# Optimization experiments

Measured on AMD Instinct MI355X. Metric: run time of the kernel, lower is better.

## Reference

```python
import jax, jax.numpy as jnp
import numpy as np

H = 768    # bert hidden size
P = 64     # num dialogue pairs
L = 2 * P  # interleaved (user,system) sequence length
C = 2      # num_classes (CRF tags)
LAM = 0.1  # lambda_mle


def setup_inputs():
    key = jax.random.key(0)
    ks = jax.random.split(key, 21)
    def rn(k, shape, s=0.05):
        return jax.random.normal(k, shape, dtype=jnp.float32) * s
    G = 4 * H
    return {
        "user_repr": rn(ks[0], (P, H), 1.0),
        "system_repr": rn(ks[1], (P, H), 1.0),
        "post_Wih0": rn(ks[2], (2, G, H)), "post_Whh0": rn(ks[3], (2, G, H)), "post_b0": rn(ks[4], (2, G)),
        "post_Wih1": rn(ks[5], (2, G, 2 * H)), "post_Whh1": rn(ks[6], (2, G, H)), "post_b1": rn(ks[7], (2, G)),
        "prior_Wih0": rn(ks[8], (2, G, H)), "prior_Whh0": rn(ks[9], (2, G, H)), "prior_b0": rn(ks[10], (2, G)),
        "prior_Wih1": rn(ks[11], (2, G, 2 * H)), "prior_Whh1": rn(ks[12], (2, G, H)), "prior_b1": rn(ks[13], (2, G)),
        "post_proj_W": rn(ks[14], (C, 2 * H)), "post_proj_b": rn(ks[15], (C,)),
        "prior_proj_W": rn(ks[16], (C, 2 * H)), "prior_proj_b": rn(ks[17], (C,)),
        "transitions": rn(ks[18], (C, C), 0.1),
        "user_I_label": jax.random.randint(ks[19], (1, P), 0, C),
        "system_I_label": jax.random.randint(ks[20], (1, P), 0, C),
    }


def _lstm_dir(x, mask, Wih, Whh, b, reverse):
    # x: [P, L, Din]; mask: [P, L] bool (True = valid step). Masked steps freeze state,
    # so each row computes the LSTM over its own prefix exactly as the per-pair loop does.
    Pn, Ln, _ = x.shape
    Hn = Whh.shape[1]
    xw = jnp.einsum('pld,gd->plg', x, Wih) + b  # [P, L, 4H] input projections (torch gate order i,f,g,o)
    def step(carry, inp):
        h, c = carry
        xw_t, m_t = inp
        gates = xw_t + h @ Whh.T
        i, f, g, o = jnp.split(gates, 4, axis=-1)
        c2 = jax.nn.sigmoid(f) * c + jax.nn.sigmoid(i) * jnp.tanh(g)
        h2 = jax.nn.sigmoid(o) * jnp.tanh(c2)
        m = m_t[:, None]
        h = jnp.where(m, h2, h)
        c = jnp.where(m, c2, c)
        return (h, c), h
    init = (jnp.zeros((Pn, Hn), x.dtype), jnp.zeros((Pn, Hn), x.dtype))
    _, hs = jax.lax.scan(step, init, (jnp.swapaxes(xw, 0, 1), mask.T), reverse=reverse)
    return jnp.swapaxes(hs, 0, 1)  # [P, L, H]


def _bilstm(x, mask, layers):
    for Wih, Whh, b in layers:
        fwd = _lstm_dir(x, mask, Wih[0], Whh[0], b[0], False)
        bwd = _lstm_dir(x, mask, Wih[1], Whh[1], b[1], True)
        x = jnp.concatenate([fwd, bwd], axis=-1)
    return x


def _forward(user_repr, system_repr,
             post_Wih0, post_Whh0, post_b0, post_Wih1, post_Whh1, post_b1,
             prior_Wih0, prior_Whh0, prior_b0, prior_Wih1, prior_Whh1, prior_b1,
             post_proj_W, post_proj_b, prior_proj_W, prior_proj_b, transitions, labs):
    seq = jnp.stack([user_repr, system_repr], axis=1).reshape(L, H)  # interleaved u0,s0,u1,s1,...
    l = 2 * (jnp.arange(P) + 1)                 # prefix length per pair
    t = jnp.arange(L)
    mask = t[None, :] < l[:, None]              # [P, L]
    xb = jnp.broadcast_to(seq[None], (P, L, H))
    # posterior branch: biLSTM over each prefix, then emissions
    post_out = _bilstm(xb, mask, [(post_Wih0, post_Whh0, post_b0), (post_Wih1, post_Whh1, post_b1)])
    em = post_out @ post_proj_W.T + post_proj_b  # [P, L, C]
    mf = mask.astype(em.dtype)
    # CRF gold score per pair
    e_lab = jnp.take_along_axis(em, jnp.broadcast_to(labs[None, :, None], (P, L, 1)), axis=2)[..., 0]
    trans_step = transitions[labs[:-1], labs[1:]]  # [L-1]
    gold = (e_lab * mf).sum(1) + (trans_step[None, :] * mf[:, 1:]).sum(1)
    # CRF forward algorithm (log partition), masked scan over time
    def fstep(alpha, inp):
        em_t, m_t = inp  # [P, C], [P]
        new = jax.nn.logsumexp(alpha[:, :, None] + transitions[None, :, :] + em_t[:, None, :], axis=1)
        return jnp.where(m_t[:, None], new, alpha), None
    alpha, _ = jax.lax.scan(fstep, em[:, 0, :], (jnp.swapaxes(em[:, 1:, :], 0, 1), mask[:, 1:].T))
    total = jax.nn.logsumexp(alpha, axis=1)
    loss_crf = jnp.mean(total - gold)
    # prior branch: prefix minus last token, take last valid hidden
    mask_p = t[None, :] < (l - 1)[:, None]
    prior_out = _bilstm(xb, mask_p, [(prior_Wih0, prior_Whh0, prior_b0), (prior_Wih1, prior_Whh1, prior_b1)])
    prior_last = jnp.take_along_axis(prior_out, jnp.broadcast_to((l - 2)[:, None, None], (P, 1, 2 * H)), axis=1)[:, 0, :]
    prior_emis = prior_last @ prior_proj_W.T + prior_proj_b  # [P, C]
    post_last = jnp.take_along_axis(em, jnp.broadcast_to((l - 1)[:, None, None], (P, 1, C)), axis=1)[:, 0, :]
    loss_mle = jnp.mean((prior_emis - jax.lax.stop_gradient(post_last)) ** 2)
    return loss_crf, loss_mle, loss_crf + LAM * loss_mle


def reference(user_repr, system_repr,
              post_Wih0, post_Whh0, post_b0, post_Wih1, post_Whh1, post_b1,
              prior_Wih0, prior_Whh0, prior_b0, prior_Wih1, prior_Whh1, prior_b1,
              post_proj_W, post_proj_b, prior_proj_W, prior_proj_b, transitions,
              user_I_label, system_I_label):
    labs = jnp.stack([user_I_label[0], system_I_label[0]], axis=1).reshape(L)
    return _forward(user_repr, system_repr,
                    post_Wih0, post_Whh0, post_b0, post_Wih1, post_Whh1, post_b1,
                    prior_Wih0, prior_Whh0, prior_b0, prior_Wih1, prior_Whh1, prior_b1,
                    post_proj_W, post_proj_b, prior_proj_W, prior_proj_b, transitions, labs)
```

## Files before the change

kernel.cpp:

```cpp
#include <hip/hip_runtime.h>


typedef short v8s __attribute__((ext_vector_type(8)));
typedef float v4f __attribute__((ext_vector_type(4)));
typedef unsigned short u16;

#define MFMA(a, b, c) __builtin_amdgcn_mfma_f32_16x16x32_bf16((a), (b), (c), 0, 0, 0)

static constexpr size_t WMAT    = (size_t)96 * 3072 * 8;
static constexpr size_t SLOT64  = (size_t)96 * 64 * 8;
static constexpr size_t SLOT16  = (size_t)96 * 16 * 8;
static constexpr size_t SLOT128 = (size_t)96 * 128 * 8;

static constexpr size_t OFF_CALL = 0;
static constexpr size_t SZ_CALL  = (size_t)8 * 64 * 768 * 4;
static constexpr size_t OFF_EM   = OFF_CALL + SZ_CALL;
static constexpr size_t SZ_EM    = (size_t)2 * 64 * 128 * 2 * 4;
static constexpr size_t OFF_XW0  = OFF_EM + SZ_EM;
static constexpr size_t SZ_XW    = (size_t)4 * 128 * 3072 * 4;
static constexpr size_t OFF_XW1  = OFF_XW0 + SZ_XW;
static constexpr size_t OFF_SEQ  = OFF_XW1 + SZ_XW;
static constexpr size_t SZ_SEQ   = (size_t)96 * 128 * 8 * 2;
static constexpr size_t OFF_LABS = OFF_SEQ + SZ_SEQ;
static constexpr size_t SZ_LABS  = 512;
static constexpr size_t OFF_W0   = OFF_LABS + SZ_LABS;
static constexpr size_t SZ_W4    = (size_t)4 * WMAT * 2;
static constexpr size_t OFF_W1X  = OFF_W0 + SZ_W4;
static constexpr size_t OFF_W1R  = OFF_W1X + SZ_W4;
static constexpr size_t OFF_F0   = OFF_W1R + SZ_W4;
static constexpr size_t SZ_F0    = (size_t)2 * 129 * SLOT16 * 2;
static constexpr size_t OFF_H0F  = OFF_F0 + SZ_F0;
static constexpr size_t SZ_H0F   = (size_t)2 * SLOT128 * 2;
static constexpr size_t OFF_B0   = OFF_H0F + SZ_H0F;
static constexpr size_t SZ_S64   = (size_t)2 * 129 * SLOT64 * 2;
static constexpr size_t OFF_F1   = OFF_B0 + SZ_S64;
static constexpr size_t OFF_B1   = OFF_F1 + SZ_S64;
static constexpr size_t WS_NEED  = OFF_B1 + SZ_S64;

static __device__ __forceinline__ u16 f2b(float f) {
  unsigned int u = __float_as_uint(f);
  unsigned int r = (u + 0x7FFFu + ((u >> 16) & 1u)) >> 16;
  return (u16)r;
}
static __device__ __forceinline__ float b2f(u16 u) {
  return __uint_as_float(((unsigned int)u) << 16);
}
static __device__ __forceinline__ float sigf(float x) {
  return 1.0f / (1.0f + __expf(-x));
}
static __device__ __forceinline__ float tanhfast(float x) {
  return 1.0f - 2.0f / (__expf(2.0f * x) + 1.0f);
}
static __device__ __forceinline__ float lse2(float a, float b) {
  float mx = fmaxf(a, b);
  return mx + __logf(__expf(a - mx) + __expf(b - mx));
}

static __device__ __forceinline__ void stage_w(const u16* mat, int kb0, int jb, u16* lds) {
  const int4* src = (const int4*)mat;
  int4* dst = (int4*)lds;
  int tid = threadIdx.x;
#pragma unroll
  for (int it = 0; it < 12; ++it) {
    int ck = it * 256 + tid;
    int kb = ck >> 6;
    int r = ck & 63;
    int g = (r >> 4) * 768 + jb + (r & 15);
    dst[ck] = src[(size_t)(kb0 + kb) * 3072 + g];
  }
}

__global__ void init_zero(float* c_all, u16* f0a, u16* f0b, u16* b0a, u16* b0b,
                          u16* f1a, u16* f1b, u16* b1a, u16* b1b) {
  int idx = blockIdx.x * 256 + threadIdx.x;
  c_all[idx] = 0.0f;
  if (idx < (int)SLOT16) { f0a[idx] = 0; f0b[idx] = 0; }
  if (idx < (int)SLOT64) {
    b0a[idx] = 0; b0b[idx] = 0;
    f1a[idx] = 0; f1b[idx] = 0;
    b1a[idx] = 0; b1b[idx] = 0;
  }
}

__global__ void build_seq(const float* user, const float* sysr, const int* ulab,
                          const int* slab, u16* seqkp, int* labs) {
  int idx = blockIdx.x * 256 + threadIdx.x;
  int t = idx / 768;
  int hh = idx - t * 768;
  float v = (t & 1) ? sysr[(t >> 1) * 768 + hh] : user[(t >> 1) * 768 + hh];
  seqkp[((size_t)(hh >> 3) * 128 + t) * 8 + (hh & 7)] = f2b(v);
  if (idx < 128) labs[idx] = (idx & 1) ? slab[idx >> 1] : ulab[idx >> 1];
}

__global__ void cvt_w(const float* postWhh0, const float* priWhh0,
                      const float* postWih1, const float* priWih1,
                      const float* postWhh1, const float* priWhh1,
                      u16* W0kp, u16* W1xkp, u16* W1rkp) {
  int mat = blockIdx.y;
  int grp = mat >> 2;
  int sub = mat & 3;
  int m = sub >> 1;
  int dirw = sub & 1;
  const float* src;
  int stride, coff;
  u16* dstb;
  if (grp == 0)      { src = m ? priWhh0 : postWhh0; stride = 768;  coff = 0;   dstb = W0kp; }
  else if (grp == 1) { src = m ? priWih1 : postWih1; stride = 1536; coff = 768; dstb = W1xkp; }
  else               { src = m ? priWhh1 : postWhh1; stride = 768;  coff = 0;   dstb = W1rkp; }
  src += (size_t)dirw * 3072 * stride;
  int cid = blockIdx.x * 256 + threadIdx.x;
  int g = cid / 96;
  int kb = cid - g * 96;
  const float* s = src + (size_t)g * stride + coff + (size_t)kb * 8;
  union { u16 h[8]; int4 v; } u;
#pragma unroll
  for (int j = 0; j < 8; ++j) u.h[j] = f2b(s[j]);
  ((int4*)(dstb + (size_t)sub * WMAT))[(size_t)kb * 3072 + g] = u.v;
}

__global__ void __launch_bounds__(256) xw_gemm(const u16* Akp, unsigned long long Astride,
                                               const float* Wm0, const float* Wm1, int wstride,
                                               const float* bm0, const float* bm1, float* out) {
  __shared__ u16 lds[48 * 64 * 8];
  int tid = threadIdx.x;
  int lane = tid & 63;
  int wave = tid >> 6;
  int md = blockIdx.y;
  int m = md >> 1;
  int dir = md & 1;
  const u16* A = Akp + (size_t)m * Astride;
  const float* W = (m ? Wm1 : Wm0) + (size_t)dir * 3072 * wstride;
  const float* b = (m ? bm1 : bm0) + dir * 3072;
  int g0 = blockIdx.x * 64;
  int quad = lane >> 4, l15 = lane & 15;
  v4f acc[2][4];
#pragma unroll
  for (int a = 0; a < 2; ++a)
#pragma unroll
    for (int nt = 0; nt < 4; ++nt) acc[a][nt] = (v4f){0.f, 0.f, 0.f, 0.f};

  for (int hfl = 0; hfl < 2; ++hfl) {
    if (hfl) __syncthreads();
    for (int it = 0; it < 12; ++it) {
      int ck = it * 256 + tid;
      int kb = ck >> 6;
      int r = ck & 63;
      int g = g0 + r;
      const float* s = W + (size_t)g * wstride + (size_t)(hfl * 48 + kb) * 8;
      union { u16 h[8]; int4 v; } u;
#pragma unroll
      for (int j = 0; j < 8; ++j) u.h[j] = f2b(s[j]);
      *(int4*)(lds + (size_t)ck * 8) = u.v;
    }
    __syncthreads();
    for (int lt = 0; lt < 12; ++lt) {
      int kblk = (hfl * 12 + lt) * 4 + quad;
      v8s a0 = ((const v8s*)A)[(size_t)kblk * 128 + (wave * 2 + 0) * 16 + l15];
      v8s a1 = ((const v8s*)A)[(size_t)kblk * 128 + (wave * 2 + 1) * 16 + l15];
#pragma unroll
      for (int nt = 0; nt < 4; ++nt) {
        v8s bb = *(const v8s*)(lds + ((size_t)((lt * 4 + quad) * 64) + nt * 16 + l15) * 8);
        acc[0][nt] = MFMA(a0, bb, acc[0][nt]);
        acc[1][nt] = MFMA(a1, bb, acc[1][nt]);
      }
    }
  }
#pragma unroll
  for (int a = 0; a < 2; ++a)
#pragma unroll
    for (int nt = 0; nt < 4; ++nt) {
      int g = g0 + nt * 16 + l15;
      float bv = b[g];
#pragma unroll
      for (int r = 0; r < 4; ++r) {
        int trow = (wave * 2 + a) * 16 + quad * 4 + r;
        out[(size_t)(md * 128 + trow) * 3072 + g] = acc[a][nt][r] + bv;
      }
    }
}

__global__ void __launch_bounds__(256) stepA_k(int t, const u16* W0kp, const float* xw0,
                                               u16* B0, u16* F0, u16* h0f, float* c_all) {
  __shared__ u16 lds[48 * 64 * 8];
  int tid = threadIdx.x;
  int lane = tid & 63;
  int wave = tid >> 6;
  int c = blockIdx.y;
  int isf = c >> 1;
  int m = c & 1;
  int dir = isf ? 0 : 1;
  int jb = blockIdx.x * 16;
  int quad = lane >> 4, l15 = lane & 15;
  const u16* mat = W0kp + (size_t)(m * 2 + dir) * WMAT;
  const u16* Asrc;
  int R, rowbase;
  if (isf) { Asrc = F0 + (size_t)(m * 129 + t) * SLOT16; R = 16; rowbase = 0; }
  else     { Asrc = B0 + (size_t)(m * 129 + t + 1) * SLOT64; R = 64; rowbase = wave * 16; }
  v4f acc[4];
#pragma unroll
  for (int gt = 0; gt < 4; ++gt) acc[gt] = (v4f){0.f, 0.f, 0.f, 0.f};
  bool docomp = (!isf) || (wave == 0);

  for (int hfl = 0; hfl < 2; ++hfl) {
    if (hfl) __syncthreads();
    stage_w(mat, hfl * 48, jb, lds);
    __syncthreads();
    if (docomp) {
      for (int lt = 0; lt < 12; ++lt) {
        int kblk = hfl * 48 + lt * 4 + quad;
        v8s a = ((const v8s*)Asrc)[(size_t)kblk * R + rowbase + l15];
#pragma unroll
        for (int gt = 0; gt < 4; ++gt) {
          v8s bb = *(const v8s*)(lds + ((size_t)((lt * 4 + quad) * 4 + gt) * 16 + l15) * 8);
          acc[gt] = MFMA(a, bb, acc[gt]);
        }
      }
    }
  }
  if (!docomp) return;

  int j = jb + l15;
  const float* xw = xw0 + (size_t)((m * 2 + dir) * 128 + t) * 3072;
  float xi = xw[j], xf = xw[768 + j], xg = xw[1536 + j], xo = xw[2304 + j];
  float* cs = c_all + (size_t)c * 64 * 768;
  if (!isf) {
    u16* dst = B0 + (size_t)(m * 129 + t) * SLOT64;
#pragma unroll
    for (int r = 0; r < 4; ++r) {
      int p = wave * 16 + quad * 4 + r;
      float gi = sigf(acc[0][r] + xi), gf = sigf(acc[1][r] + xf);
      float gg = tanhfast(acc[2][r] + xg), go = sigf(acc[3][r] + xo);
      float cold = cs[(size_t)p * 768 + j];
      float cn = gf * cold + gi * gg;
      float hn = go * tanhfast(cn);
      int lenp = 2 * p + 2 - m;
      bool act = t < lenp;
      float ce = act ? cn : 0.f;
      float he = act ? hn : 0.f;
      cs[(size_t)p * 768 + j] = ce;
      dst[((size_t)(j >> 3) * 64 + p) * 8 + (j & 7)] = f2b(he);
    }
  } else {
    if (quad == 0) {
      float gi = sigf(acc[0][0] + xi), gf = sigf(acc[1][0] + xf);
      float gg = tanhfast(acc[2][0] + xg), go = sigf(acc[3][0] + xo);
      float cold = cs[j];
      float cn = gf * cold + gi * gg;
      float hn = go * tanhfast(cn);
      cs[j] = cn;
      F0[(size_t)(m * 129 + t + 1) * SLOT16 + ((size_t)(j >> 3) * 16) * 8 + (j & 7)] = f2b(hn);
      h0f[(size_t)m * SLOT128 + ((size_t)(j >> 3) * 128 + t) * 8 + (j & 7)] = f2b(hn);
    }
  }
}

__global__ void __launch_bounds__(256) stepB_k(int t, const u16* W1x, const u16* W1r,
                                               const float* xw1s, const u16* B0, u16* F1,
                                               u16* B1, float* c_all) {
  __shared__ u16 lds[48 * 64 * 8];
  int tid = threadIdx.x;
  int lane = tid & 63;
  int wave = tid >> 6;
  int md = blockIdx.y;
  int m = md >> 1;
  int dir = md & 1;
  int jb = blockIdx.x * 16;
  int quad = lane >> 4, l15 = lane & 15;
  const u16* A1 = B0 + (size_t)(m * 129 + t) * SLOT64;
  const u16* A2 = dir ? (const u16*)(B1 + (size_t)(m * 129 + t + 1) * SLOT64)
                      : (const u16*)(F1 + (size_t)(m * 129 + t) * SLOT64);
  v4f acc[4];
#pragma unroll
  for (int gt = 0; gt < 4; ++gt) acc[gt] = (v4f){0.f, 0.f, 0.f, 0.f};

  for (int q = 0; q < 4; ++q) {
    if (q) __syncthreads();
    const u16* mat = (q < 2 ? W1x : W1r) + (size_t)md * WMAT;
    stage_w(mat, (q & 1) * 48, jb, lds);
    __syncthreads();
    const u16* As = (q < 2) ? A1 : A2;
    int akb0 = (q & 1) * 48;
    for (int lt = 0; lt < 12; ++lt) {
      v8s a = ((const v8s*)As)[(size_t)(akb0 + lt * 4 + quad) * 64 + wave * 16 + l15];
#pragma unroll
      for (int gt = 0; gt < 4; ++gt) {
        v8s bb = *(const v8s*)(lds + ((size_t)((lt * 4 + quad) * 4 + gt) * 16 + l15) * 8);
        acc[gt] = MFMA(a, bb, acc[gt]);
      }
    }
  }

  int j = jb + l15;
  const float* xw = xw1s + (size_t)(md * 128 + t) * 3072;
  float xi = xw[j], xf = xw[768 + j], xg = xw[1536 + j], xo = xw[2304 + j];
  float* cs = c_all + (size_t)(4 + md) * 64 * 768;
  u16* dst = dir ? (B1 + (size_t)(m * 129 + t) * SLOT64)
                 : (F1 + (size_t)(m * 129 + t + 1) * SLOT64);
  const u16* F1t = F1 + (size_t)(m * 129 + t) * SLOT64;
#pragma unroll
  for (int r = 0; r < 4; ++r) {
    int p = wave * 16 + quad * 4 + r;
    float gi = sigf(acc[0][r] + xi), gf = sigf(acc[1][r] + xf);
    float gg = tanhfast(acc[2][r] + xg), go = sigf(acc[3][r] + xo);
    float cold = cs[(size_t)p * 768 + j];
    float cn = gf * cold + gi * gg;
    float hn = go * tanhfast(cn);
    int lenp = 2 * p + 2 - m;
    bool act = t < lenp;
    float he, ce;
    if (!dir) {
      if (act) { he = hn; ce = cn; }
      else { he = b2f(F1t[((size_t)(j >> 3) * 64 + p) * 8 + (j & 7)]); ce = cold; }
    } else {
      he = act ? hn : 0.f;
      ce = act ? cn : 0.f;
    }
    cs[(size_t)p * 768 + j] = ce;
    dst[((size_t)(j >> 3) * 64 + p) * 8 + (j & 7)] = f2b(he);
  }
}

__global__ void __launch_bounds__(256) em_k(const u16* F1, const u16* B1,
                                            const float* pW0, const float* pb0,
                                            const float* pW1, const float* pb1, float* em) {
  int wid = blockIdx.x * 4 + (threadIdx.x >> 6);
  int lane = threadIdx.x & 63;
  int m = wid >> 13;
  int rem = wid & 8191;
  int p = rem >> 7;
  int t = rem & 127;
  const u16* hf = F1 + (size_t)(m * 129 + t + 1) * SLOT64;
  const u16* hb = B1 + (size_t)(m * 129 + t) * SLOT64;
  const float* Pw = m ? pW1 : pW0;
  const float* Pb = m ? pb1 : pb0;
  float s0 = 0.f, s1 = 0.f;
#pragma unroll
  for (int i = 0; i < 12; ++i) {
    int j = i * 64 + lane;
    size_t o = ((size_t)(j >> 3) * 64 + p) * 8 + (j & 7);
    float vf = b2f(hf[o]);
    float vb = b2f(hb[o]);
    s0 += Pw[j] * vf + Pw[768 + j] * vb;
    s1 += Pw[1536 + j] * vf + Pw[2304 + j] * vb;
  }
  for (int off = 32; off; off >>= 1) {
    s0 += __shfl_down(s0, off, 64);
    s1 += __shfl_down(s1, off, 64);
  }
  if (lane == 0) {
    em[((size_t)(m * 64 + p) * 128 + t) * 2 + 0] = s0 + Pb[0];
    em[((size_t)(m * 64 + p) * 128 + t) * 2 + 1] = s1 + Pb[1];
  }
}

__global__ void final_k(const float* em, const int* labs, const float* T, float* out) {
  int p = threadIdx.x;
  const float* emP = em + (size_t)p * 128 * 2;
  int lp = 2 * p + 2;
  float T00 = T[0], T01 = T[1], T10 = T[2], T11 = T[3];
  int prevlab = labs[0];
  float gold = emP[prevlab];
  for (int t = 1; t < lp; ++t) {
    int lb = labs[t];
    gold += emP[t * 2 + lb] + (prevlab ? (lb ? T11 : T10) : (lb ? T01 : T00));
    prevlab = lb;
  }
  float a0 = emP[0], a1 = emP[1];
  for (int t = 1; t < lp; ++t) {
    float n0 = lse2(a0 + T00, a1 + T10) + emP[t * 2];
    float n1 = lse2(a0 + T01, a1 + T11) + emP[t * 2 + 1];
    a0 = n0;
    a1 = n1;
  }
  float crf = lse2(a0, a1) - gold;
  const float* emR = em + (size_t)(64 + p) * 128 * 2;
  int lpr = 2 * p + 1;
  float d0 = emR[(lpr - 1) * 2 + 0] - emP[(lp - 1) * 2 + 0];
  float d1 = emR[(lpr - 1) * 2 + 1] - emP[(lp - 1) * 2 + 1];
  float mse = d0 * d0 + d1 * d1;
  for (int off = 32; off; off >>= 1) {
    crf += __shfl_down(crf, off, 64);
    mse += __shfl_down(mse, off, 64);
  }
  if (p == 0) {
    float lc = crf / 64.f;
    float lm = mse / 128.f;
    out[0] = lc;
    out[1] = lm;
    out[2] = lc + 0.1f * lm;
  }
}

extern "C" void kernel_launch(void* const* d_in, const int* in_sizes, int n_in,
                              void* d_out, int out_size, void* d_ws, size_t ws_size,
                              hipStream_t stream) {
  (void)in_sizes; (void)n_in; (void)out_size;
  if (ws_size < WS_NEED) return;

  const float* user     = (const float*)d_in[0];
  const float* sysr     = (const float*)d_in[1];
  const float* postWih0 = (const float*)d_in[2];
  const float* postWhh0 = (const float*)d_in[3];
  const float* postb0   = (const float*)d_in[4];
  const float* postWih1 = (const float*)d_in[5];
  const float* postWhh1 = (const float*)d_in[6];
  const float* postb1   = (const float*)d_in[7];
  const float* priWih0  = (const float*)d_in[8];
  const float* priWhh0  = (const float*)d_in[9];
  const float* prib0    = (const float*)d_in[10];
  const float* priWih1  = (const float*)d_in[11];
  const float* priWhh1  = (const float*)d_in[12];
  const float* prib1    = (const float*)d_in[13];
  const float* postPW   = (const float*)d_in[14];
  const float* postPb   = (const float*)d_in[15];
  const float* priPW    = (const float*)d_in[16];
  const float* priPb    = (const float*)d_in[17];
  const float* trans    = (const float*)d_in[18];
  const int*   ulab     = (const int*)d_in[19];
  const int*   slab     = (const int*)d_in[20];
  float* out = (float*)d_out;

  char* w = (char*)d_ws;
  float* c_all = (float*)(w + OFF_CALL);
  float* em    = (float*)(w + OFF_EM);
  float* xw0   = (float*)(w + OFF_XW0);
  float* xw1s  = (float*)(w + OFF_XW1);
  u16* seqkp   = (u16*)(w + OFF_SEQ);
  int* labs    = (int*)(w + OFF_LABS);
  u16* W0kp    = (u16*)(w + OFF_W0);
  u16* W1xkp   = (u16*)(w + OFF_W1X);
  u16* W1rkp   = (u16*)(w + OFF_W1R);
  u16* F0      = (u16*)(w + OFF_F0);
  u16* h0f     = (u16*)(w + OFF_H0F);
  u16* B0      = (u16*)(w + OFF_B0);
  u16* F1      = (u16*)(w + OFF_F1);
  u16* B1      = (u16*)(w + OFF_B1);

  init_zero<<<1536, 256, 0, stream>>>(
      c_all,
      F0, F0 + (size_t)129 * SLOT16,
      B0 + (size_t)128 * SLOT64, B0 + (size_t)(129 + 128) * SLOT64,
      F1, F1 + (size_t)129 * SLOT64,
      B1 + (size_t)128 * SLOT64, B1 + (size_t)(129 + 128) * SLOT64);

  build_seq<<<384, 256, 0, stream>>>(user, sysr, ulab, slab, seqkp, labs);

  cvt_w<<<dim3(1152, 12), 256, 0, stream>>>(postWhh0, priWhh0, postWih1, priWih1,
                                            postWhh1, priWhh1, W0kp, W1xkp, W1rkp);

  xw_gemm<<<dim3(48, 4), 256, 0, stream>>>(seqkp, 0ULL, postWih0, priWih0, 768,
                                           postb0, prib0, xw0);

  for (int t = 0; t < 128; ++t)
    stepA_k<<<dim3(48, 4), 256, 0, stream>>>(t, W0kp, xw0, B0, F0, h0f, c_all);

  xw_gemm<<<dim3(48, 4), 256, 0, stream>>>(h0f, (unsigned long long)SLOT128,
                                           postWih1, priWih1, 1536, postb1, prib1, xw1s);

  for (int t = 0; t < 128; ++t)
    stepB_k<<<dim3(48, 4), 256, 0, stream>>>(t, W1xkp, W1rkp, xw1s, B0, F1, B1, c_all);

  em_k<<<4096, 256, 0, stream>>>(F1, B1, postPW, postPb, priPW, priPb, em);

  final_k<<<1, 64, 0, stream>>>(em, labs, trans, out);
}
```

Measured before the change: 4.060 ms.

## Replace per-timestep LSTM kernel launches with persistent cooperative kernel and grid barriers

Replaces the 256 per-timestep kernel launches for both BiLSTM layers with one persistent cooperative kernel of 192 blocks. Each block keeps its recurrent weight slice resident in LDS and holds the cell state in registers instead of global memory. Timesteps are separated by atomic-counter group barriers, and the layer-1 input projection GEMM is folded into the same kernel. This removes launch overhead and repeated weight staging per step. The cost is spin-wait barrier overhead and a 147 KB LDS footprint, and correctness relies on all 192 blocks being co-resident.

```diff
diff --git a/kernel.cpp b/kernel.cpp
--- a/kernel.cpp
+++ b/kernel.cpp
@@ -12,9 +12,9 @@
 static constexpr size_t SLOT16  = (size_t)96 * 16 * 8;
 static constexpr size_t SLOT128 = (size_t)96 * 128 * 8;
 
-static constexpr size_t OFF_CALL = 0;
-static constexpr size_t SZ_CALL  = (size_t)8 * 64 * 768 * 4;
-static constexpr size_t OFF_EM   = OFF_CALL + SZ_CALL;
+static constexpr size_t OFF_CTR  = 0;
+static constexpr size_t SZ_CTR   = 4096;
+static constexpr size_t OFF_EM   = OFF_CTR + SZ_CTR;
 static constexpr size_t SZ_EM    = (size_t)2 * 64 * 128 * 2 * 4;
 static constexpr size_t OFF_XW0  = OFF_EM + SZ_EM;
 static constexpr size_t SZ_XW    = (size_t)4 * 128 * 3072 * 4;
@@ -37,6 +37,8 @@
 static constexpr size_t OFF_B1   = OFF_F1 + SZ_S64;
 static constexpr size_t WS_NEED  = OFF_B1 + SZ_S64;
 
+static constexpr unsigned LDS_BYTES = 147456;
+
 static __device__ __forceinline__ u16 f2b(float f) {
   unsigned int u = __float_as_uint(f);
   unsigned int r = (u + 0x7FFFu + ((u >> 16) & 1u)) >> 16;
@@ -45,9 +47,7 @@
 static __device__ __forceinline__ float b2f(u16 u) {
   return __uint_as_float(((unsigned int)u) << 16);
 }
-static __device__ __forceinline__ float sigf(float x) {
-  return 1.0f / (1.0f + __expf(-x));
-}
+static __device__ __forceinline__ float sigf(float x) { return 1.0f / (1.0f + __expf(-x)); }
 static __device__ __forceinline__ float tanhfast(float x) {
   return 1.0f - 2.0f / (__expf(2.0f * x) + 1.0f);
 }
@@ -56,30 +56,24 @@
   return mx + __logf(__expf(a - mx) + __expf(b - mx));
 }
 
-static __device__ __forceinline__ void stage_w(const u16* mat, int kb0, int jb, u16* lds) {
-  const int4* src = (const int4*)mat;
-  int4* dst = (int4*)lds;
-  int tid = threadIdx.x;
-#pragma unroll
-  for (int it = 0; it < 12; ++it) {
-    int ck = it * 256 + tid;
-    int kb = ck >> 6;
-    int r = ck & 63;
-    int g = (r >> 4) * 768 + jb + (r & 15);
-    dst[ck] = src[(size_t)(kb0 + kb) * 3072 + g];
-  }
-}
-
-__global__ void init_zero(float* c_all, u16* f0a, u16* f0b, u16* b0a, u16* b0b,
-                          u16* f1a, u16* f1b, u16* b1a, u16* b1b) {
+static __device__ __forceinline__ void gbar(unsigned* ctr, unsigned target) {
+  __syncthreads();
+  if (threadIdx.x == 0) {
+    __hip_atomic_fetch_add(ctr, 1u, __ATOMIC_RELEASE, __HIP_MEMORY_SCOPE_AGENT);
+    while (__hip_atomic_load(ctr, __ATOMIC_ACQUIRE, __HIP_MEMORY_SCOPE_AGENT) < target)
+      __builtin_amdgcn_s_sleep(1);
+  }
+  __syncthreads();
+}
+
+__global__ void init_zero(u16* f0a, u16* f0b, u16* b0a, u16* b0b,
+                          u16* f1a, u16* f1b, u16* b1a, u16* b1b, unsigned* ctrs) {
   int idx = blockIdx.x * 256 + threadIdx.x;
-  c_all[idx] = 0.0f;
+  if (idx < 1024) ctrs[idx] = 0;
   if (idx < (int)SLOT16) { f0a[idx] = 0; f0b[idx] = 0; }
-  if (idx < (int)SLOT64) {
-    b0a[idx] = 0; b0b[idx] = 0;
-    f1a[idx] = 0; f1b[idx] = 0;
-    b1a[idx] = 0; b1b[idx] = 0;
-  }
+  b0a[idx] = 0; b0b[idx] = 0;
+  f1a[idx] = 0; f1b[idx] = 0;
+  b1a[idx] = 0; b1b[idx] = 0;
 }
 
 __global__ void build_seq(const float* user, const float* sysr, const int* ulab,
@@ -118,8 +112,8 @@
   ((int4*)(dstb + (size_t)sub * WMAT))[(size_t)kb * 3072 + g] = u.v;
 }
 
-__global__ void __launch_bounds__(256) xw_gemm(const u16* Akp, unsigned long long Astride,
-                                               const float* Wm0, const float* Wm1, int wstride,
+__global__ void __launch_bounds__(256) xw_gemm(const u16* Akp,
+                                               const float* Wm0, const float* Wm1,
                                                const float* bm0, const float* bm1, float* out) {
   __shared__ u16 lds[48 * 64 * 8];
   int tid = threadIdx.x;
@@ -128,8 +122,7 @@
   int md = blockIdx.y;
   int m = md >> 1;
   int dir = md & 1;
-  const u16* A = Akp + (size_t)m * Astride;
-  const float* W = (m ? Wm1 : Wm0) + (size_t)dir * 3072 * wstride;
+  const float* W = (m ? Wm1 : Wm0) + (size_t)dir * 3072 * 768;
   const float* b = (m ? bm1 : bm0) + dir * 3072;
   int g0 = blockIdx.x * 64;
   int quad = lane >> 4, l15 = lane & 15;
@@ -145,8 +138,7 @@
       int ck = it * 256 + tid;
       int kb = ck >> 6;
       int r = ck & 63;
-      int g = g0 + r;
-      const float* s = W + (size_t)g * wstride + (size_t)(hfl * 48 + kb) * 8;
+      const float* s = W + (size_t)(g0 + r) * 768 + (size_t)(hfl * 48 + kb) * 8;
       union { u16 h[8]; int4 v; } u;
 #pragma unroll
       for (int j = 0; j < 8; ++j) u.h[j] = f2b(s[j]);
@@ -155,8 +147,8 @@
     __syncthreads();
     for (int lt = 0; lt < 12; ++lt) {
       int kblk = (hfl * 12 + lt) * 4 + quad;
-      v8s a0 = ((const v8s*)A)[(size_t)kblk * 128 + (wave * 2 + 0) * 16 + l15];
-      v8s a1 = ((const v8s*)A)[(size_t)kblk * 128 + (wave * 2 + 1) * 16 + l15];
+      v8s a0 = ((const v8s*)Akp)[(size_t)kblk * 128 + (wave * 2 + 0) * 16 + l15];
+      v8s a1 = ((const v8s*)Akp)[(size_t)kblk * 128 + (wave * 2 + 1) * 16 + l15];
 #pragma unroll
       for (int nt = 0; nt < 4; ++nt) {
         v8s bb = *(const v8s*)(lds + ((size_t)((lt * 4 + quad) * 64) + nt * 16 + l15) * 8);
@@ -179,144 +171,255 @@
     }
 }
 
-__global__ void __launch_bounds__(256) stepA_k(int t, const u16* W0kp, const float* xw0,
-                                               u16* B0, u16* F0, u16* h0f, float* c_all) {
-  __shared__ u16 lds[48 * 64 * 8];
+__global__ void __launch_bounds__(256, 1) persist_k(
+    const u16* __restrict__ W0kp, const u16* __restrict__ W1xkp,
+    const u16* __restrict__ W1rkp, const float* __restrict__ xw0,
+    const float* __restrict__ postWih1, const float* __restrict__ priWih1,
+    const float* __restrict__ postb1, const float* __restrict__ prib1,
+    u16* F0, u16* h0f, u16* B0, u16* F1, u16* B1, float* xw1s, unsigned* ctrs) {
+  extern __shared__ u16 lds[];
+  u16* stg = lds + 49152;
   int tid = threadIdx.x;
   int lane = tid & 63;
   int wave = tid >> 6;
-  int c = blockIdx.y;
-  int isf = c >> 1;
-  int m = c & 1;
-  int dir = isf ? 0 : 1;
-  int jb = blockIdx.x * 16;
+  int grp = blockIdx.x / 48;
+  int jb = (blockIdx.x % 48) * 16;
   int quad = lane >> 4, l15 = lane & 15;
-  const u16* mat = W0kp + (size_t)(m * 2 + dir) * WMAT;
-  const u16* Asrc;
-  int R, rowbase;
-  if (isf) { Asrc = F0 + (size_t)(m * 129 + t) * SLOT16; R = 16; rowbase = 0; }
-  else     { Asrc = B0 + (size_t)(m * 129 + t + 1) * SLOT64; R = 64; rowbase = wave * 16; }
-  v4f acc[4];
-#pragma unroll
-  for (int gt = 0; gt < 4; ++gt) acc[gt] = (v4f){0.f, 0.f, 0.f, 0.f};
-  bool docomp = (!isf) || (wave == 0);
-
-  for (int hfl = 0; hfl < 2; ++hfl) {
-    if (hfl) __syncthreads();
-    stage_w(mat, hfl * 48, jb, lds);
+  int j = jb + l15;
+
+  {
+    int isf = grp >> 1;
+    int m = grp & 1;
+    int dir = isf ? 0 : 1;
+    const int4* wsrc = (const int4*)(W0kp + (size_t)(m * 2 + dir) * WMAT);
+    int4* dres = (int4*)lds;
+    for (int it = 0; it < 24; ++it) {
+      int ck = it * 256 + tid;
+      int kb = ck >> 6;
+      int r = ck & 63;
+      dres[ck] = wsrc[(size_t)kb * 3072 + (r >> 4) * 768 + jb + (r & 15)];
+    }
     __syncthreads();
-    if (docomp) {
-      for (int lt = 0; lt < 12; ++lt) {
-        int kblk = hfl * 48 + lt * 4 + quad;
-        v8s a = ((const v8s*)Asrc)[(size_t)kblk * R + rowbase + l15];
-#pragma unroll
-        for (int gt = 0; gt < 4; ++gt) {
-          v8s bb = *(const v8s*)(lds + ((size_t)((lt * 4 + quad) * 4 + gt) * 16 + l15) * 8);
-          acc[gt] = MFMA(a, bb, acc[gt]);
-        }
-      }
-    }
-  }
-  if (!docomp) return;
-
-  int j = jb + l15;
-  const float* xw = xw0 + (size_t)((m * 2 + dir) * 128 + t) * 3072;
-  float xi = xw[j], xf = xw[768 + j], xg = xw[1536 + j], xo = xw[2304 + j];
-  float* cs = c_all + (size_t)c * 64 * 768;
-  if (!isf) {
-    u16* dst = B0 + (size_t)(m * 129 + t) * SLOT64;
-#pragma unroll
-    for (int r = 0; r < 4; ++r) {
-      int p = wave * 16 + quad * 4 + r;
-      float gi = sigf(acc[0][r] + xi), gf = sigf(acc[1][r] + xf);
-      float gg = tanhfast(acc[2][r] + xg), go = sigf(acc[3][r] + xo);
-      float cold = cs[(size_t)p * 768 + j];
-      float cn = gf * cold + gi * gg;
-      float hn = go * tanhfast(cn);
-      int lenp = 2 * p + 2 - m;
-      bool act = t < lenp;
-      float ce = act ? cn : 0.f;
-      float he = act ? hn : 0.f;
-      cs[(size_t)p * 768 + j] = ce;
-      dst[((size_t)(j >> 3) * 64 + p) * 8 + (j & 7)] = f2b(he);
-    }
-  } else {
-    if (quad == 0) {
-      float gi = sigf(acc[0][0] + xi), gf = sigf(acc[1][0] + xf);
-      float gg = tanhfast(acc[2][0] + xg), go = sigf(acc[3][0] + xo);
-      float cold = cs[j];
-      float cn = gf * cold + gi * gg;
-      float hn = go * tanhfast(cn);
-      cs[j] = cn;
-      F0[(size_t)(m * 129 + t + 1) * SLOT16 + ((size_t)(j >> 3) * 16) * 8 + (j & 7)] = f2b(hn);
-      h0f[(size_t)m * SLOT128 + ((size_t)(j >> 3) * 128 + t) * 8 + (j & 7)] = f2b(hn);
-    }
-  }
-}
-
-__global__ void __launch_bounds__(256) stepB_k(int t, const u16* W1x, const u16* W1r,
-                                               const float* xw1s, const u16* B0, u16* F1,
-                                               u16* B1, float* c_all) {
-  __shared__ u16 lds[48 * 64 * 8];
-  int tid = threadIdx.x;
-  int lane = tid & 63;
-  int wave = tid >> 6;
-  int md = blockIdx.y;
+
+    float cr[4] = {0.f, 0.f, 0.f, 0.f};
+    float hr[4] = {0.f, 0.f, 0.f, 0.f};
+    unsigned* ctrA = ctrs + grp * 32;
+    const float* xwbase = xw0 + (size_t)(m * 2 + dir) * 128 * 3072;
+
+#pragma unroll 1
+    for (int s = 0; s < 128; ++s) {
+      int t = isf ? s : 127 - s;
+      if (!isf) {
+        const v8s* A = (const v8s*)(B0 + (size_t)(m * 129 + t + 1) * SLOT64);
+        v4f acc[4];
+#pragma unroll
+        for (int gt = 0; gt < 4; ++gt) acc[gt] = (v4f){0.f, 0.f, 0.f, 0.f};
+#pragma unroll 4
+        for (int lt = 0; lt < 24; ++lt) {
+          int kblk = lt * 4 + quad;
+          v8s a = A[(size_t)kblk * 64 + wave * 16 + l15];
+#pragma unroll
+          for (int gt = 0; gt < 4; ++gt) {
+            v8s bb = *(const v8s*)(lds + ((size_t)(kblk * 64 + gt * 16 + l15)) * 8);
+            acc[gt] = MFMA(a, bb, acc[gt]);
+          }
+        }
+        const float* xw = xwbase + (size_t)t * 3072;
+        float xi = xw[j], xf = xw[768 + j], xg = xw[1536 + j], xo = xw[2304 + j];
+        u16* dst = B0 + (size_t)(m * 129 + t) * SLOT64;
+#pragma unroll
+        for (int r = 0; r < 4; ++r) {
+          int p = wave * 16 + quad * 4 + r;
+          float gi = sigf(acc[0][r] + xi), gf = sigf(acc[1][r] + xf);
+          float gg = tanhfast(acc[2][r] + xg), go = sigf(acc[3][r] + xo);
+          float cn = gf * cr[r] + gi * gg;
+          float hn = go * tanhfast(cn);
+          bool act = t < (2 * p + 2 - m);
+          cr[r] = act ? cn : cr[r];
+          float he = act ? hn : hr[r];
+          hr[r] = he;
+          dst[((size_t)(j >> 3) * 64 + p) * 8 + (j & 7)] = f2b(he);
+        }
+      } else {
+        if (wave == 0) {
+          const v8s* A = (const v8s*)(F0 + (size_t)(m * 129 + t) * SLOT16);
+          v4f acc[4];
+#pragma unroll
+          for (int gt = 0; gt < 4; ++gt) acc[gt] = (v4f){0.f, 0.f, 0.f, 0.f};
+#pragma unroll 4
+          for (int lt = 0; lt < 24; ++lt) {
+            int kblk = lt * 4 + quad;
+            v8s a = A[(size_t)kblk * 16 + l15];
+#pragma unroll
+            for (int gt = 0; gt < 4; ++gt) {
+              v8s bb = *(const v8s*)(lds + ((size_t)(kblk * 64 + gt * 16 + l15)) * 8);
+              acc[gt] = MFMA(a, bb, acc[gt]);
+            }
+          }
+          if (quad == 0) {
+            const float* xw = xwbase + (size_t)t * 3072;
+            float gi = sigf(acc[0][0] + xw[j]), gf = sigf(acc[1][0] + xw[768 + j]);
+            float gg = tanhfast(acc[2][0] + xw[1536 + j]), go = sigf(acc[3][0] + xw[2304 + j]);
+            float cn = gf * cr[0] + gi * gg;
+            float hn = go * tanhfast(cn);
+            cr[0] = cn;
+            F0[(size_t)(m * 129 + t + 1) * SLOT16 + ((size_t)(j >> 3) * 16) * 8 + (j & 7)] = f2b(hn);
+            h0f[(size_t)m * SLOT128 + ((size_t)(j >> 3) * 128 + t) * 8 + (j & 7)] = f2b(hn);
+          }
+        }
+      }
+      gbar(ctrA, (unsigned)(s + 1) * 48);
+    }
+  }
+
+  gbar(ctrs + 8 * 32, 192);
+
+  int md = grp;
   int m = md >> 1;
   int dir = md & 1;
-  int jb = blockIdx.x * 16;
-  int quad = lane >> 4, l15 = lane & 15;
-  const u16* A1 = B0 + (size_t)(m * 129 + t) * SLOT64;
-  const u16* A2 = dir ? (const u16*)(B1 + (size_t)(m * 129 + t + 1) * SLOT64)
-                      : (const u16*)(F1 + (size_t)(m * 129 + t) * SLOT64);
-  v4f acc[4];
-#pragma unroll
-  for (int gt = 0; gt < 4; ++gt) acc[gt] = (v4f){0.f, 0.f, 0.f, 0.f};
-
-  for (int q = 0; q < 4; ++q) {
-    if (q) __syncthreads();
-    const u16* mat = (q < 2 ? W1x : W1r) + (size_t)md * WMAT;
-    stage_w(mat, (q & 1) * 48, jb, lds);
+  {
+    const float* Wsrc = (m ? priWih1 : postWih1) + (size_t)dir * 3072 * 1536;
+    for (int it = 0; it < 24; ++it) {
+      int ck = it * 256 + tid;
+      int kb = ck >> 6;
+      int r = ck & 63;
+      const float* sp = Wsrc + (size_t)((r >> 4) * 768 + jb + (r & 15)) * 1536 + (size_t)kb * 8;
+      union { u16 h[8]; int4 v; } u;
+#pragma unroll
+      for (int q = 0; q < 8; ++q) u.h[q] = f2b(sp[q]);
+      ((int4*)lds)[ck] = u.v;
+    }
     __syncthreads();
-    const u16* As = (q < 2) ? A1 : A2;
-    int akb0 = (q & 1) * 48;
-    for (int lt = 0; lt < 12; ++lt) {
-      v8s a = ((const v8s*)As)[(size_t)(akb0 + lt * 4 + quad) * 64 + wave * 16 + l15];
+    const v8s* A = (const v8s*)(h0f + (size_t)m * SLOT128);
+    const float* bsl = (m ? prib1 : postb1) + dir * 3072;
+    v4f acc2[2][4];
+#pragma unroll
+    for (int a = 0; a < 2; ++a)
+#pragma unroll
+      for (int gt = 0; gt < 4; ++gt) acc2[a][gt] = (v4f){0.f, 0.f, 0.f, 0.f};
+    for (int lt = 0; lt < 24; ++lt) {
+      int kblk = lt * 4 + quad;
+      v8s a0 = A[(size_t)kblk * 128 + (wave * 2 + 0) * 16 + l15];
+      v8s a1 = A[(size_t)kblk * 128 + (wave * 2 + 1) * 16 + l15];
 #pragma unroll
       for (int gt = 0; gt < 4; ++gt) {
-        v8s bb = *(const v8s*)(lds + ((size_t)((lt * 4 + quad) * 4 + gt) * 16 + l15) * 8);
-        acc[gt] = MFMA(a, bb, acc[gt]);
-      }
-    }
-  }
-
-  int j = jb + l15;
-  const float* xw = xw1s + (size_t)(md * 128 + t) * 3072;
-  float xi = xw[j], xf = xw[768 + j], xg = xw[1536 + j], xo = xw[2304 + j];
-  float* cs = c_all + (size_t)(4 + md) * 64 * 768;
-  u16* dst = dir ? (B1 + (size_t)(m * 129 + t) * SLOT64)
-                 : (F1 + (size_t)(m * 129 + t + 1) * SLOT64);
-  const u16* F1t = F1 + (size_t)(m * 129 + t) * SLOT64;
-#pragma unroll
-  for (int r = 0; r < 4; ++r) {
-    int p = wave * 16 + quad * 4 + r;
-    float gi = sigf(acc[0][r] + xi), gf = sigf(acc[1][r] + xf);
-    float gg = tanhfast(acc[2][r] + xg), go = sigf(acc[3][r] + xo);
-    float cold = cs[(size_t)p * 768 + j];
-    float cn = gf * cold + gi * gg;
-    float hn = go * tanhfast(cn);
-    int lenp = 2 * p + 2 - m;
-    bool act = t < lenp;
-    float he, ce;
-    if (!dir) {
-      if (act) { he = hn; ce = cn; }
-      else { he = b2f(F1t[((size_t)(j >> 3) * 64 + p) * 8 + (j & 7)]); ce = cold; }
-    } else {
-      he = act ? hn : 0.f;
-      ce = act ? cn : 0.f;
-    }
-    cs[(size_t)p * 768 + j] = ce;
-    dst[((size_t)(j >> 3) * 64 + p) * 8 + (j & 7)] = f2b(he);
+        v8s bb = *(const v8s*)(lds + ((size_t)(kblk * 64 + gt * 16 + l15)) * 8);
+        acc2[0][gt] = MFMA(a0, bb, acc2[0][gt]);
+        acc2[1][gt] = MFMA(a1, bb, acc2[1][gt]);
+      }
+    }
+#pragma unroll
+    for (int a = 0; a < 2; ++a)
+#pragma unroll
+      for (int gt = 0; gt < 4; ++gt) {
+        int gG = gt * 768 + jb + l15;
+        float bv = bsl[gG];
+#pragma unroll
+        for (int r = 0; r < 4; ++r) {
+          int trow = (wave * 2 + a) * 16 + quad * 4 + r;
+          xw1s[((size_t)md * 128 + trow) * 3072 + gG] = acc2[a][gt][r] + bv;
+        }
+      }
+    __syncthreads();
+  }
+
+  {
+    const int4* wr = (const int4*)(W1rkp + (size_t)md * WMAT);
+    int4* dres = (int4*)lds;
+    for (int it = 0; it < 24; ++it) {
+      int ck = it * 256 + tid;
+      int kb = ck >> 6;
+      int r = ck & 63;
+      dres[ck] = wr[(size_t)kb * 3072 + (r >> 4) * 768 + jb + (r & 15)];
+    }
+    __syncthreads();
+
+    const int4* wx = (const int4*)(W1xkp + (size_t)md * WMAT);
+    unsigned* ctrB = ctrs + (4 + md) * 32;
+    float cr[4] = {0.f, 0.f, 0.f, 0.f};
+    float hr[4] = {0.f, 0.f, 0.f, 0.f};
+
+#pragma unroll 1
+    for (int s = 0; s < 128; ++s) {
+      int t = dir ? 127 - s : s;
+      const v8s* A1 = (const v8s*)(B0 + (size_t)(m * 129 + t) * SLOT64);
+      const v8s* A2 = (const v8s*)(dir ? (B1 + (size_t)(m * 129 + t + 1) * SLOT64)
+                                       : (F1 + (size_t)(m * 129 + t) * SLOT64));
+      v4f acc[4];
+#pragma unroll
+      for (int gt = 0; gt < 4; ++gt) acc[gt] = (v4f){0.f, 0.f, 0.f, 0.f};
+
+      int4 rw[12];
+#pragma unroll
+      for (int it = 0; it < 12; ++it) {
+        int ck = it * 256 + tid;
+        int kb = ck >> 6;
+        int r = ck & 63;
+        rw[it] = wx[(size_t)kb * 3072 + (r >> 4) * 768 + jb + (r & 15)];
+      }
+#pragma unroll 4
+      for (int lt = 0; lt < 24; ++lt) {
+        int kblk = lt * 4 + quad;
+        v8s a = A2[(size_t)kblk * 64 + wave * 16 + l15];
+#pragma unroll
+        for (int gt = 0; gt < 4; ++gt) {
+          v8s bb = *(const v8s*)(lds + ((size_t)(kblk * 64 + gt * 16 + l15)) * 8);
+          acc[gt] = MFMA(a, bb, acc[gt]);
+        }
+      }
+#pragma unroll
+      for (int it = 0; it < 12; ++it) ((int4*)stg)[it * 256 + tid] = rw[it];
+      __syncthreads();
+#pragma unroll
+      for (int it = 0; it < 12; ++it) {
+        int ck = it * 256 + tid;
+        int kb = 48 + (ck >> 6);
+        int r = ck & 63;
+        rw[it] = wx[(size_t)kb * 3072 + (r >> 4) * 768 + jb + (r & 15)];
+      }
+#pragma unroll 4
+      for (int lt = 0; lt < 12; ++lt) {
+        int kl = lt * 4 + quad;
+        v8s a = A1[(size_t)kl * 64 + wave * 16 + l15];
+#pragma unroll
+        for (int gt = 0; gt < 4; ++gt) {
+          v8s bb = *(const v8s*)(stg + ((size_t)(kl * 64 + gt * 16 + l15)) * 8);
+          acc[gt] = MFMA(a, bb, acc[gt]);
+        }
+      }
+      __syncthreads();
+#pragma unroll
+      for (int it = 0; it < 12; ++it) ((int4*)stg)[it * 256 + tid] = rw[it];
+      __syncthreads();
+#pragma unroll 4
+      for (int lt = 0; lt < 12; ++lt) {
+        int kl = lt * 4 + quad;
+        v8s a = A1[(size_t)(48 + kl) * 64 + wave * 16 + l15];
+#pragma unroll
+        for (int gt = 0; gt < 4; ++gt) {
+          v8s bb = *(const v8s*)(stg + ((size_t)(kl * 64 + gt * 16 + l15)) * 8);
+          acc[gt] = MFMA(a, bb, acc[gt]);
+        }
+      }
+      const float* xw = xw1s + ((size_t)md * 128 + t) * 3072;
+      float xi = xw[j], xf = xw[768 + j], xg = xw[1536 + j], xo = xw[2304 + j];
+      u16* dst = dir ? (B1 + (size_t)(m * 129 + t) * SLOT64)
+                     : (F1 + (size_t)(m * 129 + t + 1) * SLOT64);
+#pragma unroll
+      for (int r = 0; r < 4; ++r) {
+        int p = wave * 16 + quad * 4 + r;
+        float gi = sigf(acc[0][r] + xi), gf = sigf(acc[1][r] + xf);
+        float gg = tanhfast(acc[2][r] + xg), go = sigf(acc[3][r] + xo);
+        float cn = gf * cr[r] + gi * gg;
+        float hn = go * tanhfast(cn);
+        bool act = t < (2 * p + 2 - m);
+        cr[r] = act ? cn : cr[r];
+        float he = act ? hn : hr[r];
+        hr[r] = he;
+        dst[((size_t)(j >> 3) * 64 + p) * 8 + (j & 7)] = f2b(he);
+      }
+      gbar(ctrB, (unsigned)(s + 1) * 48);
+    }
   }
 }
 
@@ -421,7 +524,7 @@
   float* out = (float*)d_out;
 
   char* w = (char*)d_ws;
-  float* c_all = (float*)(w + OFF_CALL);
+  unsigned* ctrs = (unsigned*)(w + OFF_CTR);
   float* em    = (float*)(w + OFF_EM);
   float* xw0   = (float*)(w + OFF_XW0);
   float* xw1s  = (float*)(w + OFF_XW1);
@@ -436,29 +539,33 @@
   u16* F1      = (u16*)(w + OFF_F1);
   u16* B1      = (u16*)(w + OFF_B1);
 
-  init_zero<<<1536, 256, 0, stream>>>(
-      c_all,
+  init_zero<<<192, 256, 0, stream>>>(
       F0, F0 + (size_t)129 * SLOT16,
       B0 + (size_t)128 * SLOT64, B0 + (size_t)(129 + 128) * SLOT64,
       F1, F1 + (size_t)129 * SLOT64,
-      B1 + (size_t)128 * SLOT64, B1 + (size_t)(129 + 128) * SLOT64);
+      B1 + (size_t)128 * SLOT64, B1 + (size_t)(129 + 128) * SLOT64, ctrs);
 
   build_seq<<<384, 256, 0, stream>>>(user, sysr, ulab, slab, seqkp, labs);
 
   cvt_w<<<dim3(1152, 12), 256, 0, stream>>>(postWhh0, priWhh0, postWih1, priWih1,
                                             postWhh1, priWhh1, W0kp, W1xkp, W1rkp);
 
-  xw_gemm<<<dim3(48, 4), 256, 0, stream>>>(seqkp, 0ULL, postWih0, priWih0, 768,
-                                           postb0, prib0, xw0);
-
-  for (int t = 0; t < 128; ++t)
-    stepA_k<<<dim3(48, 4), 256, 0, stream>>>(t, W0kp, xw0, B0, F0, h0f, c_all);
-
-  xw_gemm<<<dim3(48, 4), 256, 0, stream>>>(h0f, (unsigned long long)SLOT128,
-                                           postWih1, priWih1, 1536, postb1, prib1, xw1s);
-
-  for (int t = 0; t < 128; ++t)
-    stepB_k<<<dim3(48, 4), 256, 0, stream>>>(t, W1xkp, W1rkp, xw1s, B0, F1, B1, c_all);
+  xw_gemm<<<dim3(48, 4), 256, 0, stream>>>(seqkp, postWih0, priWih0, postb0, prib0, xw0);
+
+  {
+    const u16* a0 = W0kp; const u16* a1 = W1xkp; const u16* a2 = W1rkp;
+    const float* a3 = xw0;
+    void* args[] = {(void*)&a0, (void*)&a1, (void*)&a2, (void*)&a3,
+                    (void*)&postWih1, (void*)&priWih1, (void*)&postb1, (void*)&prib1,
+                    (void*)&F0, (void*)&h0f, (void*)&B0, (void*)&F1, (void*)&B1,
+                    (void*)&xw1s, (void*)&ctrs};
+    hipError_t e = hipLaunchCooperativeKernel((const void*)persist_k, dim3(192), dim3(256),
+                                              args, LDS_BYTES, stream);
+    if (e != hipSuccess) {
+      persist_k<<<192, 256, LDS_BYTES, stream>>>(W0kp, W1xkp, W1rkp, xw0, postWih1, priWih1,
+                                                 postb1, prib1, F0, h0f, B0, F1, B1, xw1s, ctrs);
+    }
+  }
 
   em_k<<<4096, 256, 0, stream>>>(F1, B1, postPW, postPb, priPW, priPb, em);
 
```

Result: slower. 6.017 ms (+48.2%).
